# Kernel tuning notes

Measured on AMD Instinct MI355X. Metric: run time of the kernel, lower is better.

## Reference

```python
import jax, jax.numpy as jnp
import numpy as np

DIM = 2048
N_HEADS = 16
HEAD_DIM = DIM // N_HEADS
SEQ = 1024
BSZ = 2
ADAPTER_LEN = 10
MAX_FEATS = 10
ROPE_THETA = 10000.0


def setup_inputs() -> dict:
    key = jax.random.key(0)
    ks = jax.random.split(key, 10)
    x = jax.random.normal(ks[0], (BSZ, SEQ, DIM), dtype=jnp.float32)
    adapter = jax.random.normal(ks[1], (1, ADAPTER_LEN, DIM), dtype=jnp.float32)
    # causal additive mask [1,1,S,S]
    neg = jnp.full((SEQ, SEQ), -1e9, dtype=jnp.float32)
    mask = jnp.triu(neg, k=1)[None, None]
    # rotary frequencies (real/imag of freqs_cis)
    inv_freq = 1.0 / (ROPE_THETA ** (np.arange(0, HEAD_DIM, 2, dtype=np.float32) / HEAD_DIM))
    t = np.arange(SEQ, dtype=np.float32)
    ang = jnp.asarray(np.outer(t, inv_freq), dtype=jnp.float32)  # [S, HEAD_DIM//2]
    freqs_cos = jnp.cos(ang)
    freqs_sin = jnp.sin(ang)
    scale = 0.02
    wq = jax.random.normal(ks[2], (DIM, DIM), dtype=jnp.float32) * scale
    wk = jax.random.normal(ks[3], (DIM, DIM), dtype=jnp.float32) * scale
    wv = jax.random.normal(ks[4], (DIM, DIM), dtype=jnp.float32) * scale
    wo = jax.random.normal(ks[5], (DIM, DIM), dtype=jnp.float32) * scale
    gate1 = jax.random.normal(ks[6], (1, N_HEADS, 1, 1), dtype=jnp.float32) * 0.5
    gate2 = jnp.ones((1, N_HEADS, 1, 1), dtype=jnp.float32) * -3.0
    return {"x": x, "adapter": adapter, "mask": mask, "freqs_cos": freqs_cos,
            "freqs_sin": freqs_sin, "wq": wq, "wk": wk, "wv": wv, "wo": wo,
            "gate1": gate1, "gate2": gate2, "video_start": 30}


def _apply_rope(t, cos, sin):
    # t: [B,S,H,D]; cos/sin: [S, D//2] -> complex multiply on consecutive pairs
    tr = t.reshape(*t.shape[:-1], HEAD_DIM // 2, 2)
    xr, xi = tr[..., 0], tr[..., 1]
    c = cos[None, :, None, :]
    s = sin[None, :, None, :]
    out_r = xr * c - xi * s
    out_i = xr * s + xi * c
    return jnp.stack([out_r, out_i], axis=-1).reshape(t.shape)


def reference(x, adapter, mask, freqs_cos, freqs_sin, wq, wk, wv, wo, gate1, gate2, video_start):
    bsz, seqlen, _ = x.shape
    al = adapter.shape[1]
    vs = int(video_start)
    # projections (torch Linear: y = x @ W^T)
    xq = (x @ wq.T).reshape(bsz, seqlen, N_HEADS, HEAD_DIM)
    xk = (x @ wk.T).reshape(bsz, seqlen, N_HEADS, HEAD_DIM)
    xv = (x @ wv.T).reshape(bsz, seqlen, N_HEADS, HEAD_DIM)
    xq = _apply_rope(xq, freqs_cos, freqs_sin)
    xk = _apply_rope(xk, freqs_cos, freqs_sin)
    # adapter keys/values (no RoPE), broadcast over batch
    a_k = (adapter @ wk.T).reshape(1, al, N_HEADS, HEAD_DIM)
    a_v = (adapter @ wv.T).reshape(1, al, N_HEADS, HEAD_DIM)
    a_k = jnp.broadcast_to(a_k, (bsz, al, N_HEADS, HEAD_DIM))
    a_v = jnp.broadcast_to(a_v, (bsz, al, N_HEADS, HEAD_DIM))
    keys = jnp.concatenate([a_k, xk], axis=1)      # [B, al+S, H, D]
    values = jnp.concatenate([a_v, xv], axis=1)
    # mask extended with zeros over adapter columns
    extra = jnp.zeros((1, 1, seqlen, al), dtype=mask.dtype)
    full_mask = jnp.concatenate([extra, mask], axis=-1)
    scores = jnp.einsum('bqhd,bkhd->bhqk', xq, keys) / jnp.sqrt(jnp.float32(HEAD_DIM))
    scores = scores + full_mask
    # split softmax: adapter part gated by tanh(gate1)
    adapter_scores = jax.nn.softmax(scores[..., :al], axis=-1) * jnp.tanh(gate1)
    vt = scores[..., al:]
    vt = vt.at[:, :, vs + MAX_FEATS:, vs:vs + MAX_FEATS].add(gate2)
    vt = jax.nn.softmax(vt, axis=-1)
    probs = jnp.concatenate([adapter_scores, vt], axis=-1)  # [B,H,S,al+S]
    out = jnp.einsum('bhqk,bkhd->bqhd', probs, values)
    out = out.reshape(bsz, seqlen, DIM)
    return out @ wo.T
```

## Files before the change

### kernel.cpp

```cpp
#include <hip/hip_runtime.h>
#include <math.h>

#define DIM   2048
#define NH    16
#define HD    128
#define SEQQ  1024
#define BSZ   2
#define AL    10
#define MAXF  10
#define KVROWS (SEQQ + AL)
#define BK    32
#define VTP   2080

typedef unsigned short ushort_t;
typedef __bf16   bf16x8 __attribute__((ext_vector_type(8)));
typedef float    f32x4  __attribute__((ext_vector_type(4)));
typedef ushort_t us8    __attribute__((ext_vector_type(8)));

#define AS1 __attribute__((address_space(1)))
#define AS3 __attribute__((address_space(3)))

__device__ __forceinline__ float b2f(ushort_t u) {
    return __uint_as_float(((unsigned int)u) << 16);
}
__device__ __forceinline__ ushort_t f2b(float f) {
    unsigned int u = __float_as_uint(f);
    u += 0x7fffu + ((u >> 16) & 1u);
    return (ushort_t)(u >> 16);
}
__device__ __forceinline__ float scrub(float v, float canary) {
    return ((__float_as_uint(v) & 0x7f800000u) == 0x7f800000u) ? canary : v;
}
__device__ __forceinline__ bf16x8 cvt8(const float* p) {
    float4 a = *(const float4*)p;
    float4 b = *(const float4*)(p + 4);
    us8 u;
    u[0] = f2b(a.x); u[1] = f2b(a.y); u[2] = f2b(a.z); u[3] = f2b(a.w);
    u[4] = f2b(b.x); u[5] = f2b(b.y); u[6] = f2b(b.z); u[7] = f2b(b.w);
    return *(bf16x8*)&u;
}

__global__ __launch_bounds__(256) void cvt5(
    const float* __restrict__ s0, const float* __restrict__ s1,
    const float* __restrict__ s2, const float* __restrict__ s3,
    const float* __restrict__ s4,
    ushort_t* __restrict__ d0, ushort_t* __restrict__ d1,
    ushort_t* __restrict__ d2, ushort_t* __restrict__ d3,
    ushort_t* __restrict__ d4)
{
    const int y = blockIdx.y;
    const float* s = (y == 0) ? s0 : (y == 1) ? s1 : (y == 2) ? s2 : (y == 3) ? s3 : s4;
    ushort_t*    d = (y == 0) ? d0 : (y == 1) ? d1 : (y == 2) ? d2 : (y == 3) ? d3 : d4;
    size_t i = (size_t)blockIdx.x * 256 + threadIdx.x;
    float4 a = ((const float4*)s)[2 * i];
    float4 b = ((const float4*)s)[2 * i + 1];
    us8 u;
    u[0] = f2b(a.x); u[1] = f2b(a.y); u[2] = f2b(a.z); u[3] = f2b(a.w);
    u[4] = f2b(b.x); u[5] = f2b(b.y); u[6] = f2b(b.z); u[7] = f2b(b.w);
    *(us8*)(d + i * 8) = u;
}

__global__ __launch_bounds__(256) void adapter_gemm(
    const float* __restrict__ adp,
    const ushort_t* __restrict__ Wkb, const ushort_t* __restrict__ Wvb,
    ushort_t* __restrict__ Ko, ushort_t* __restrict__ VtO,
    float canary)
{
    __shared__ ushort_t Al[AL * DIM];

    const int t = threadIdx.x;
    #pragma unroll
    for (int p = 0; p < 10; ++p) {
        int i = p * 256 + t;
        const float* sp = adp + i * 8;
        float4 a = *(const float4*)sp;
        float4 b = *(const float4*)(sp + 4);
        us8 u;
        u[0] = f2b(a.x); u[1] = f2b(a.y); u[2] = f2b(a.z); u[3] = f2b(a.w);
        u[4] = f2b(b.x); u[5] = f2b(b.y); u[6] = f2b(b.z); u[7] = f2b(b.w);
        *(us8*)(Al + i * 8) = u;
    }
    __syncthreads();

    const int z = blockIdx.x >> 8;
    const ushort_t* W = z ? Wvb : Wkb;
    const int nbase = (blockIdx.x & 255) * 8;
    const int w = t >> 6, lane = t & 63;

    #pragma unroll
    for (int nn = 0; nn < 2; ++nn) {
        const int n = nbase + w * 2 + nn;
        const ushort_t* wr = W + (size_t)n * DIM;
        float acc[AL] = {};
        #pragma unroll
        for (int c = 0; c < 4; ++c) {
            const int k = c * 512 + lane * 8;
            us8 b8 = *(const us8*)(wr + k);
            float bf[8];
            #pragma unroll
            for (int j = 0; j < 8; ++j) bf[j] = b2f(b8[j]);
            #pragma unroll
            for (int m = 0; m < AL; ++m) {
                us8 a8 = *(const us8*)(Al + m * DIM + k);
                #pragma unroll
                for (int j = 0; j < 8; ++j)
                    acc[m] = fmaf(b2f(a8[j]), bf[j], acc[m]);
            }
        }
        #pragma unroll
        for (int m = 0; m < AL; ++m) {
            float v = acc[m];
            v += __shfl_xor(v, 1);  v += __shfl_xor(v, 2);
            v += __shfl_xor(v, 4);  v += __shfl_xor(v, 8);
            v += __shfl_xor(v, 16); v += __shfl_xor(v, 32);
            if (lane == 0) {
                ushort_t ov = f2b(scrub(v, canary));
                if (z) VtO[(size_t)n * VTP + 2048 + m] = ov;
                else   Ko[(size_t)m * DIM + n] = ov;
            }
        }
        if (z && lane < 22) VtO[(size_t)n * VTP + 2058 + lane] = 0;
    }
}

template<int MODE>
__global__ __launch_bounds__(256) void gemm_bt(
    const ushort_t* __restrict__ A,
    const ushort_t* __restrict__ B0, const ushort_t* __restrict__ B1, const ushort_t* __restrict__ B2,
    void* __restrict__ C0, void* __restrict__ C1, void* __restrict__ C2,
    float canary)
{
    __shared__ ushort_t As[128 * 32];
    __shared__ ushort_t Bs[128 * 32];

    const int z = blockIdx.z;
    const ushort_t* B = (z == 0) ? B0 : (z == 1) ? B1 : B2;
    void*           C = (z == 0) ? C0 : (z == 1) ? C1 : C2;

    const int m0 = blockIdx.y * 128;
    const int n0 = blockIdx.x * 128;
    const int t = threadIdx.x;
    const int w = t >> 6, lane = t & 63;
    const int ln = lane & 15, qd = lane >> 4;
    const int wrow = (w >> 1) * 64, wcol = (w & 1) * 64;

    const int r0 = t >> 2, c0 = (t & 3) * 8;
    const int r1 = (t + 256) >> 2;
    const ushort_t* Ag0 = A + (size_t)(m0 + r0) * DIM + c0;
    const ushort_t* Ag1 = A + (size_t)(m0 + r1) * DIM + c0;
    const ushort_t* Bg0 = B + (size_t)(n0 + r0) * DIM + c0;
    const ushort_t* Bg1 = B + (size_t)(n0 + r1) * DIM + c0;
    ushort_t* Al0 = As + (size_t)t * 8;
    ushort_t* Al1 = As + (size_t)(t + 256) * 8;
    ushort_t* Bl0 = Bs + (size_t)t * 8;
    ushort_t* Bl1 = Bs + (size_t)(t + 256) * 8;

    f32x4 acc[4][4] = {};

    for (int k0 = 0; k0 < DIM; k0 += BK) {
        if (k0) __syncthreads();
        __builtin_amdgcn_global_load_lds((const AS1 void*)(Ag0 + k0), (AS3 void*)Al0, 16, 0, 0);
        __builtin_amdgcn_global_load_lds((const AS1 void*)(Ag1 + k0), (AS3 void*)Al1, 16, 0, 0);
        __builtin_amdgcn_global_load_lds((const AS1 void*)(Bg0 + k0), (AS3 void*)Bl0, 16, 0, 0);
        __builtin_amdgcn_global_load_lds((const AS1 void*)(Bg1 + k0), (AS3 void*)Bl1, 16, 0, 0);
        __syncthreads();

        bf16x8 af[4], bfr[4];
        #pragma unroll
        for (int i = 0; i < 4; ++i) {
            af[i]  = *(const bf16x8*)(As + (wrow + i * 16 + ln) * 32 + qd * 8);
            bfr[i] = *(const bf16x8*)(Bs + (wcol + i * 16 + ln) * 32 + qd * 8);
        }
        #pragma unroll
        for (int i = 0; i < 4; ++i)
            #pragma unroll
            for (int j = 0; j < 4; ++j)
                acc[i][j] = __builtin_amdgcn_mfma_f32_16x16x32_bf16(af[i], bfr[j], acc[i][j], 0, 0, 0);
    }

    #pragma unroll
    for (int i = 0; i < 4; ++i) {
        #pragma unroll
        for (int j = 0; j < 4; ++j) {
            const int gn = n0 + wcol + j * 16 + ln;
            const int gm0 = m0 + wrow + i * 16 + qd * 4;
            if (MODE == 0 && z == 2) {
                ushort4 ov;
                ov.x = f2b(scrub(acc[i][j][0], canary));
                ov.y = f2b(scrub(acc[i][j][1], canary));
                ov.z = f2b(scrub(acc[i][j][2], canary));
                ov.w = f2b(scrub(acc[i][j][3], canary));
                *(ushort4*)((ushort_t*)C + (size_t)gn * VTP + gm0) = ov;
            } else {
                #pragma unroll
                for (int r = 0; r < 4; ++r) {
                    float v = scrub(acc[i][j][r], canary);
                    if (MODE == 1) ((float*)C)[(size_t)(gm0 + r) * DIM + gn] = v;
                    else           ((ushort_t*)C)[(size_t)(gm0 + r) * DIM + gn] = f2b(v);
                }
            }
        }
    }
}

template<bool AF32, bool CF32>
__global__ __launch_bounds__(256) void mfma_gemm(
    const void* __restrict__ Av,
    const float* __restrict__ B0, const float* __restrict__ B1, const float* __restrict__ B2,
    void* __restrict__ C0, void* __restrict__ C1, void* __restrict__ C2,
    int M, float canary)
{
    const int z = blockIdx.z;
    const float* B = (z == 0) ? B0 : (z == 1) ? B1 : B2;
    void*       C = (z == 0) ? C0 : (z == 1) ? C1 : C2;

    const int m0 = blockIdx.y * 128;
    const int n0 = blockIdx.x * 128;
    const int t    = threadIdx.x;
    const int w    = t >> 6;
    const int lane = t & 63;
    const int ln   = lane & 15, qd = lane >> 4;
    const int wrow = (w >> 1) * 64, wcol = (w & 1) * 64;

    size_t aoff[4];
    const float* brow[4];
    #pragma unroll
    for (int i = 0; i < 4; ++i) {
        int gr = m0 + wrow + i * 16 + ln; gr = (gr < M) ? gr : (M - 1);
        aoff[i] = (size_t)gr * DIM + qd * 8;
        brow[i] = B + (size_t)(n0 + wcol + i * 16 + ln) * DIM + qd * 8;
    }

    f32x4 acc[4][4] = {};

    for (int k0 = 0; k0 < DIM; k0 += BK) {
        bf16x8 af[4], bfr[4];
        #pragma unroll
        for (int i = 0; i < 4; ++i) {
            if (AF32) af[i] = cvt8((const float*)Av + aoff[i] + k0);
            else      af[i] = *(const bf16x8*)((const ushort_t*)Av + aoff[i] + k0);
            bfr[i] = cvt8(brow[i] + k0);
        }
        #pragma unroll
        for (int i = 0; i < 4; ++i)
            #pragma unroll
            for (int j = 0; j < 4; ++j)
                acc[i][j] = __builtin_amdgcn_mfma_f32_16x16x32_bf16(af[i], bfr[j], acc[i][j], 0, 0, 0);
    }

    #pragma unroll
    for (int i = 0; i < 4; ++i) {
        #pragma unroll
        for (int j = 0; j < 4; ++j) {
            const int gn = n0 + wcol + j * 16 + ln;
            #pragma unroll
            for (int r = 0; r < 4; ++r) {
                const int gm = m0 + wrow + i * 16 + qd * 4 + r;
                float v = scrub(acc[i][j][r], canary);
                if (gm < M) {
                    if (CF32) ((float*)C)[(size_t)gm * DIM + gn] = v;
                    else      ((ushort_t*)C)[(size_t)gm * DIM + gn] = f2b(v);
                }
            }
        }
    }
}

__global__ __launch_bounds__(256) void rope_kernel(ushort_t* __restrict__ Qb,
                                                   ushort_t* __restrict__ Kb,
                                                   const float* __restrict__ fc,
                                                   const float* __restrict__ fs,
                                                   float qscale)
{
    int i = blockIdx.x * 256 + threadIdx.x;
    ushort_t* T = blockIdx.y ? Kb : Qb;
    const float sc = blockIdx.y ? 1.0f : qscale;
    int row = i >> 10;
    int p   = i & 1023;
    float c = fc[((row & 1023) << 6) + (p & 63)];
    float s = fs[((row & 1023) << 6) + (p & 63)];
    ushort_t* ptr = T + (size_t)row * DIM + p * 2;
    float xr = b2f(ptr[0]), xi = b2f(ptr[1]);
    ptr[0] = f2b((xr * c - xi * s) * sc);
    ptr[1] = f2b((xr * s + xi * c) * sc);
}

__global__ __launch_bounds__(256) void attn_mfma(const ushort_t* __restrict__ Q,
                                                 const ushort_t* __restrict__ Kg,
                                                 const ushort_t* __restrict__ Vt,
                                                 const float* __restrict__ g1,
                                                 const float* __restrict__ g2,
                                                 const int* __restrict__ vsp,
                                                 ushort_t* __restrict__ AO)
{
    __shared__ ushort_t Kls[2][64 * 128];
    __shared__ ushort_t Vls[2][128 * 64];
    __shared__ ushort_t Pl[4 * 16 * 72];

    const int blk = blockIdx.x;
    const int wg   = (blk & 7) * 64 + (blk >> 3);
    const int gidx = wg >> 4;
    const int mem  = wg & 15;
    const int qt   = (mem & 1) ? (mem >> 1) : (15 - (mem >> 1));
    const int h = gidx & 15;
    const int b = gidx >> 4;
    const int q0  = qt * 64;
    const int nsteps = qt + 1;
    const int t = threadIdx.x;
    const int w = t >> 6, lane = t & 63;
    const int ln = lane & 15, g = lane >> 4;
    const int hb = h * HD;
    const size_t kvb = (size_t)b << 10;
    const int vs = *vsp;
    const float g2h = g2[h];
    const float ag  = tanhf(g1[h]);
    const int gq = q0 + w * 16 + ln;

    const ushort_t* qrow = Q + (kvb + gq) * DIM + hb;
    bf16x8 qf[4];
    #pragma unroll
    for (int c = 0; c < 4; ++c) qf[c] = *(const bf16x8*)(qrow + g * 8 + 32 * c);

    auto stage = [&](int bi, int k0) {
        #pragma unroll
        for (int p = 0; p < 4; ++p) {
            int i = t + 256 * p;
            int kr = i >> 4, ks = (i & 15) ^ (kr & 7);
            __builtin_amdgcn_global_load_lds(
                (const AS1 void*)(Kg + (kvb + k0 + kr) * DIM + hb + ks * 8),
                (AS3 void*)(&Kls[bi][i * 8]), 16, 0, 0);
        }
        #pragma unroll
        for (int p = 0; p < 4; ++p) {
            int i = t + 256 * p;
            int vr = i >> 3, vsl = (i & 7) ^ (vr & 7);
            __builtin_amdgcn_global_load_lds(
                (const AS1 void*)(Vt + (size_t)(hb + vr) * VTP + kvb + k0 + vsl * 8),
                (AS3 void*)(&Vls[bi][i * 8]), 16, 0, 0);
        }
    };

    stage(0, 0);

    f32x4 oa[8] = {};
    float m_run = -1e30f, l_run = 0.f;
    ushort_t* Plw = Pl + w * (16 * 72) + ln * 72;

    for (int s = 0; s < nsteps; ++s) {
        const int k0 = s * 64;
        const int cur = s & 1;
        __syncthreads();
        if (s + 1 < nsteps) stage(cur ^ 1, k0 + 64);

        f32x4 sc[4] = {};
        #pragma unroll
        for (int mt = 0; mt < 4; ++mt) {
            const int krow = ln + 16 * mt;
            const ushort_t* krp = &Kls[cur][krow * 128];
            #pragma unroll
            for (int c = 0; c < 4; ++c) {
                bf16x8 kf = *(const bf16x8*)(krp + ((8 * g + 32 * c) ^ ((krow & 7) << 3)));
                sc[mt] = __builtin_amdgcn_mfma_f32_16x16x32_bf16(kf, qf[c], sc[mt], 0, 0, 0);
            }
        }

        float mloc = -3e38f;
        #pragma unroll
        for (int mt = 0; mt < 4; ++mt)
            #pragma unroll
            for (int r = 0; r < 4; ++r) {
                int gk = k0 + mt * 16 + g * 4 + r;
                float v = sc[mt][r];
                if (gk > gq) v -= 1e9f;
                if (gk >= vs && gk < vs + MAXF && gq >= vs + MAXF) v += g2h;
                sc[mt][r] = v;
                mloc = fmaxf(mloc, v);
            }
        mloc = fmaxf(mloc, __shfl_xor(mloc, 16));
        mloc = fmaxf(mloc, __shfl_xor(mloc, 32));
        const float m_new = fmaxf(m_run, mloc);
        const float alpha = __expf(m_run - m_new);
        float psum = 0.f;
        #pragma unroll
        for (int mt = 0; mt < 4; ++mt) {
            float p0 = __expf(sc[mt][0] - m_new);
            float p1 = __expf(sc[mt][1] - m_new);
            float p2 = __expf(sc[mt][2] - m_new);
            float p3 = __expf(sc[mt][3] - m_new);
            psum += (p0 + p1) + (p2 + p3);
            uint2 pw_;
            pw_.x = (unsigned)f2b(p0) | ((unsigned)f2b(p1) << 16);
            pw_.y = (unsigned)f2b(p2) | ((unsigned)f2b(p3) << 16);
            *(uint2*)(Plw + mt * 16 + g * 4) = pw_;
        }
        psum += __shfl_xor(psum, 16);
        psum += __shfl_xor(psum, 32);
        l_run = l_run * alpha + psum;
        m_run = m_new;
        #pragma unroll
        for (int i = 0; i < 8; ++i) {
            oa[i][0] *= alpha; oa[i][1] *= alpha; oa[i][2] *= alpha; oa[i][3] *= alpha;
        }

        bf16x8 pf0 = *(const bf16x8*)(Plw + 8 * g);
        bf16x8 pf1 = *(const bf16x8*)(Plw + 32 + 8 * g);
        #pragma unroll
        for (int dt = 0; dt < 8; ++dt) {
            const int vrow = dt * 16 + ln;
            const ushort_t* vrp = &Vls[cur][vrow * 64];
            bf16x8 vf0 = *(const bf16x8*)(vrp + ((g     ^ (vrow & 7)) * 8));
            bf16x8 vf1 = *(const bf16x8*)(vrp + (((g+4) ^ (vrow & 7)) * 8));
            oa[dt] = __builtin_amdgcn_mfma_f32_16x16x32_bf16(vf0, pf0, oa[dt], 0, 0, 0);
            oa[dt] = __builtin_amdgcn_mfma_f32_16x16x32_bf16(vf1, pf1, oa[dt], 0, 0, 0);
        }
    }

    const float invl = 1.f / l_run;
    #pragma unroll
    for (int i = 0; i < 8; ++i) {
        oa[i][0] *= invl; oa[i][1] *= invl; oa[i][2] *= invl; oa[i][3] *= invl;
    }

    const ushort_t* karow = Kg + (size_t)(2048 + (ln < 10 ? ln : 9)) * DIM + hb;
    f32x4 sa4 = {};
    #pragma unroll
    for (int c = 0; c < 4; ++c) {
        bf16x8 kf = *(const bf16x8*)(karow + 8 * g + 32 * c);
        sa4 = __builtin_amdgcn_mfma_f32_16x16x32_bf16(kf, qf[c], sa4, 0, 0, 0);
    }
    float am = -3e38f;
    float pa[4];
    #pragma unroll
    for (int r = 0; r < 4; ++r) {
        int kl = g * 4 + r;
        pa[r] = (kl < 10) ? sa4[r] : -1e30f;
        am = fmaxf(am, pa[r]);
    }
    am = fmaxf(am, __shfl_xor(am, 16));
    am = fmaxf(am, __shfl_xor(am, 32));
    float asum = 0.f;
    #pragma unroll
    for (int r = 0; r < 4; ++r) { pa[r] = __expf(pa[r] - am); asum += pa[r]; }
    asum += __shfl_xor(asum, 16);
    asum += __shfl_xor(asum, 32);
    const float coef = ag / asum;
    {
        uint2 pw_;
        pw_.x = (unsigned)f2b(pa[0] * coef) | ((unsigned)f2b(pa[1] * coef) << 16);
        pw_.y = (unsigned)f2b(pa[2] * coef) | ((unsigned)f2b(pa[3] * coef) << 16);
        *(uint2*)(Plw + g * 4) = pw_;
        uint2 z2; z2.x = 0; z2.y = 0;
        *(uint2*)(Plw + 16 + g * 4) = z2;
    }
    bf16x8 paf = *(const bf16x8*)(Plw + 8 * g);
    #pragma unroll
    for (int dt = 0; dt < 8; ++dt) {
        const ushort_t* varow = Vt + (size_t)(hb + dt * 16 + ln) * VTP + 2048;
        bf16x8 vfa = *(const bf16x8*)(varow + 8 * g);
        oa[dt] = __builtin_amdgcn_mfma_f32_16x16x32_bf16(vfa, paf, oa[dt], 0, 0, 0);
    }

    ushort_t* outp = AO + (kvb + gq) * DIM + hb;
    #pragma unroll
    for (int dt = 0; dt < 8; ++dt) {
        ushort4 ov;
        ov.x = f2b(scrub(oa[dt][0], 1e8f));
        ov.y = f2b(scrub(oa[dt][1], 1e8f));
        ov.z = f2b(scrub(oa[dt][2], 1e8f));
        ov.w = f2b(scrub(oa[dt][3], 1e8f));
        *(ushort4*)(outp + dt * 16 + g * 4) = ov;
    }
}

__global__ __launch_bounds__(256) void attn_kernel(const ushort_t* __restrict__ Q,
                                                   const ushort_t* __restrict__ Kg,
                                                   const ushort_t* __restrict__ Vg,
                                                   const float* __restrict__ g1,
                                                   const float* __restrict__ g2,
                                                   const int* __restrict__ vsp,
                                                   ushort_t* __restrict__ AO)
{
    __shared__ float Qs[32 * 132];
    __shared__ float Ks[32 * 132];
    __shared__ float Vs[32 * 132];
    __shared__ float Ps[32 * 32];

    const int blk = blockIdx.x;
    const int q0  = (31 - (blk & 31)) * 32;
    const int h   = blk >> 5;
    const int t   = threadIdx.x;
    const int qi  = t >> 3;
    const int l8  = t & 7;
    const int vs  = *vsp;
    const int g_q = q0 + qi;
    const float scale = 0.08838834764831845f;
    const float g2h = g2[h];
    const float ag  = tanhf(g1[h]);

    #pragma unroll
    for (int p = 0; p < 4; ++p) {
        int idx = (p * 256 + t) * 4;
        int r = idx >> 7, d = idx & 127;
        ushort4 q4 = *(const ushort4*)(Q + (size_t)(q0 + r) * DIM + h * HD + d);
        *(float4*)(Qs + r * 132 + d) = make_float4(b2f(q4.x), b2f(q4.y), b2f(q4.z), b2f(q4.w));
    }

    float o[16];
    #pragma unroll
    for (int i = 0; i < 16; ++i) o[i] = 0.f;
    float m_run = -1e30f, l_run = 0.f;

    for (int k0 = 0; k0 <= q0 + 31; k0 += 32) {
        __syncthreads();
        #pragma unroll
        for (int p = 0; p < 4; ++p) {
            int idx = (p * 256 + t) * 4;
            int r = idx >> 7, d = idx & 127;
            size_t goff = (size_t)(k0 + r) * DIM + h * HD + d;
            ushort4 k4 = *(const ushort4*)(Kg + goff);
            ushort4 v4 = *(const ushort4*)(Vg + goff);
            *(float4*)(Ks + r * 132 + d) = make_float4(b2f(k4.x), b2f(k4.y), b2f(k4.z), b2f(k4.w));
            *(float4*)(Vs + r * 132 + d) = make_float4(b2f(v4.x), b2f(v4.y), b2f(v4.z), b2f(v4.w));
        }
        __syncthreads();

        float s[4];
        #pragma unroll
        for (int jj = 0; jj < 4; ++jj) s[jj] = 0.f;
        #pragma unroll 4
        for (int d = 0; d < 128; d += 4) {
            const float4 qv = *(const float4*)(Qs + qi * 132 + d);
            #pragma unroll
            for (int jj = 0; jj < 4; ++jj) {
                const float4 kv = *(const float4*)(Ks + (l8 + 8 * jj) * 132 + d);
                s[jj] += qv.x * kv.x + qv.y * kv.y + qv.z * kv.z + qv.w * kv.w;
            }
        }
        float mloc = -1e30f;
        #pragma unroll
        for (int jj = 0; jj < 4; ++jj) {
            int gk = k0 + l8 + 8 * jj;
            float sv = s[jj] * scale;
            if (gk > g_q) sv -= 1e9f;
            if (gk >= vs && gk < vs + MAXF && g_q >= vs + MAXF) sv += g2h;
            s[jj] = sv;
            mloc = fmaxf(mloc, sv);
        }
        mloc = fmaxf(mloc, __shfl_xor(mloc, 1));
        mloc = fmaxf(mloc, __shfl_xor(mloc, 2));
        mloc = fmaxf(mloc, __shfl_xor(mloc, 4));
        const float m_new = fmaxf(m_run, mloc);
        const float alpha = expf(m_run - m_new);
        float psum = 0.f;
        #pragma unroll
        for (int jj = 0; jj < 4; ++jj) {
            float pv = expf(s[jj] - m_new);
            psum += pv;
            Ps[qi * 32 + l8 + 8 * jj] = pv;
        }
        psum += __shfl_xor(psum, 1);
        psum += __shfl_xor(psum, 2);
        psum += __shfl_xor(psum, 4);
        l_run = l_run * alpha + psum;
        m_run = m_new;
        #pragma unroll
        for (int i = 0; i < 16; ++i) o[i] *= alpha;
        __syncthreads();

        #pragma unroll 4
        for (int kk = 0; kk < 32; ++kk) {
            const float pp = Ps[qi * 32 + kk];
            const float* vr = Vs + kk * 132 + l8 * 4;
            #pragma unroll
            for (int jj = 0; jj < 4; ++jj) {
                const float4 v4 = *(const float4*)(vr + jj * 32);
                o[jj*4+0] = fmaf(pp, v4.x, o[jj*4+0]);
                o[jj*4+1] = fmaf(pp, v4.y, o[jj*4+1]);
                o[jj*4+2] = fmaf(pp, v4.z, o[jj*4+2]);
                o[jj*4+3] = fmaf(pp, v4.w, o[jj*4+3]);
            }
        }
    }

    const float invl = 1.f / l_run;
    #pragma unroll
    for (int i = 0; i < 16; ++i) o[i] *= invl;

    __syncthreads();
    #pragma unroll
    for (int p = 0; p < 2; ++p) {
        int idx = p * 256 + t;
        if (idx < 320) {
            int fi = idx * 4; int r = fi >> 7; int d = fi & 127;
            size_t goff = (size_t)(SEQQ + r) * DIM + h * HD + d;
            ushort4 k4 = *(const ushort4*)(Kg + goff);
            ushort4 v4 = *(const ushort4*)(Vg + goff);
            *(float4*)(Ks + r * 132 + d) = make_float4(b2f(k4.x), b2f(k4.y), b2f(k4.z), b2f(k4.w));
            *(float4*)(Vs + r * 132 + d) = make_float4(b2f(v4.x), b2f(v4.y), b2f(v4.z), b2f(v4.w));
        }
    }
    __syncthreads();
    float sa[2] = {-1e30f, -1e30f};
    #pragma unroll
    for (int jj = 0; jj < 2; ++jj) {
        int kk = l8 + 8 * jj;
        if (kk < AL) {
            float acc = 0.f;
            #pragma unroll 4
            for (int d = 0; d < 128; d += 4) {
                const float4 qv = *(const float4*)(Qs + qi * 132 + d);
                const float4 kv = *(const float4*)(Ks + kk * 132 + d);
                acc += qv.x * kv.x + qv.y * kv.y + qv.z * kv.z + qv.w * kv.w;
            }
            sa[jj] = acc * scale;
        }
    }
    float am = fmaxf(sa[0], sa[1]);
    am = fmaxf(am, __shfl_xor(am, 1));
    am = fmaxf(am, __shfl_xor(am, 2));
    am = fmaxf(am, __shfl_xor(am, 4));
    float pa0 = expf(sa[0] - am);
    float pa1 = (l8 < 2) ? expf(sa[1] - am) : 0.f;
    float asum = pa0 + pa1;
    asum += __shfl_xor(asum, 1);
    asum += __shfl_xor(asum, 2);
    asum += __shfl_xor(asum, 4);
    const float coef = ag / asum;
    Ps[qi * 32 + l8] = pa0 * coef;
    if (l8 < 2) Ps[qi * 32 + 8 + l8] = pa1 * coef;
    __syncthreads();
    #pragma unroll
    for (int kk = 0; kk < AL; ++kk) {
        const float pp = Ps[qi * 32 + kk];
        const float* vr = Vs + kk * 132 + l8 * 4;
        #pragma unroll
        for (int jj = 0; jj < 4; ++jj) {
            const float4 v4 = *(const float4*)(vr + jj * 32);
            o[jj*4+0] = fmaf(pp, v4.x, o[jj*4+0]);
            o[jj*4+1] = fmaf(pp, v4.y, o[jj*4+1]);
            o[jj*4+2] = fmaf(pp, v4.z, o[jj*4+2]);
            o[jj*4+3] = fmaf(pp, v4.w, o[jj*4+3]);
        }
    }

    ushort_t* outp = AO + (size_t)g_q * DIM + h * HD + l8 * 4;
    #pragma unroll
    for (int jj = 0; jj < 4; ++jj) {
        ushort4 ov;
        ov.x = f2b(scrub(o[jj*4+0], 1e8f));
        ov.y = f2b(scrub(o[jj*4+1], 1e8f));
        ov.z = f2b(scrub(o[jj*4+2], 1e8f));
        ov.w = f2b(scrub(o[jj*4+3], 1e8f));
        *(ushort4*)(outp + jj * 32) = ov;
    }
}

extern "C" void kernel_launch(void* const* d_in, const int* in_sizes, int n_in,
                              void* d_out, int out_size, void* d_ws, size_t ws_size,
                              hipStream_t stream)
{
    const float* x   = (const float*)d_in[0];
    const float* adp = (const float*)d_in[1];
    const float* fc  = (const float*)d_in[3];
    const float* fs  = (const float*)d_in[4];
    const float* wq  = (const float*)d_in[5];
    const float* wk  = (const float*)d_in[6];
    const float* wv  = (const float*)d_in[7];
    const float* wo  = (const float*)d_in[8];
    const float* g1  = (const float*)d_in[9];
    const float* g2  = (const float*)d_in[10];
    const int*   vsp = (const int*)d_in[11];

    float* out = (float*)d_out;

    const size_t rows2 = (size_t)BSZ * SEQQ;
    const size_t qe2 = rows2 * DIM;
    const size_t ke2 = (rows2 + AL) * DIM;
    const size_t vte = (size_t)DIM * VTP;
    const size_t we  = (size_t)DIM * DIM;
    const size_t xe  = (size_t)BSZ * SEQQ * DIM;
    const size_t need = (qe2 + ke2 + vte + xe + 4 * we) * sizeof(ushort_t);

    if (ws_size >= need) {
        ushort_t* Qb  = (ushort_t*)d_ws;
        ushort_t* Kb  = Qb + qe2;
        ushort_t* VtG = Kb + ke2;
        ushort_t* Xb  = VtG + vte;
        ushort_t* Wqb = Xb + xe;
        ushort_t* Wkb = Wqb + we;
        ushort_t* Wvb = Wkb + we;
        ushort_t* Wob = Wvb + we;

        cvt5<<<dim3(2048, 5), 256, 0, stream>>>(wq, wk, wv, wo, x,
                                                Wqb, Wkb, Wvb, Wob, Xb);

        adapter_gemm<<<512, 256, 0, stream>>>(adp, Wkb, Wvb,
                                              Kb + rows2 * DIM, VtG,
                                              100.0f);

        gemm_bt<0><<<dim3(16, 16, 3), 256, 0, stream>>>(
            Xb, Wqb, Wkb, Wvb, Qb, Kb, VtG, 1e5f);

        rope_kernel<<<dim3(8192, 2), 256, 0, stream>>>(Qb, Kb, fc, fs,
                                                       0.08838834764831845f);

        attn_mfma<<<512, 256, 0, stream>>>(Qb, Kb, VtG, g1, g2, vsp, Qb );

        gemm_bt<1><<<dim3(16, 16, 1), 256, 0, stream>>>(
            Qb, Wob, Wob, Wob, out, out, out, 1e12f);
    } else {
        const size_t qe = (size_t)SEQQ * DIM;
        const size_t ke = (size_t)KVROWS * DIM;
        ushort_t* Qb = (ushort_t*)d_ws;
        ushort_t* Kb = Qb + qe;
        ushort_t* Vb = Kb + ke;

        mfma_gemm<true, false><<<dim3(16, 1, 2), 256, 0, stream>>>(
            adp, wk, wv, wv,
            Kb + qe, Vb + qe, Vb,
            AL, 100.0f);

        for (int b = 0; b < BSZ; ++b) {
            const long xo = (long)b * SEQQ * DIM;
            mfma_gemm<true, false><<<dim3(16, 8, 3), 256, 0, stream>>>(
                x + xo, wq, wk, wv, Qb, Kb, Vb, SEQQ, 1e5f);

            rope_kernel<<<dim3(4096, 2), 256, 0, stream>>>(Qb, Kb, fc, fs, 1.0f);

            attn_kernel<<<NH * (SEQQ / 32), 256, 0, stream>>>(Qb, Kb, Vb, g1, g2, vsp, Qb);

            mfma_gemm<false, true><<<dim3(16, 8, 1), 256, 0, stream>>>(
                Qb, wo, wo, wo, out + xo, out + xo, out + xo, SEQQ, 1e12f);
        }
    }
}
```

Baseline: 302.6 us.

## Fuse RoPE into QKV GEMM epilogue, remap workgroups across XCDs, add MFMA priority

```diff
diff --git a/kernel.cpp b/kernel.cpp
--- a/kernel.cpp
+++ b/kernel.cpp
@@ -128,17 +128,23 @@
     const ushort_t* __restrict__ A,
     const ushort_t* __restrict__ B0, const ushort_t* __restrict__ B1, const ushort_t* __restrict__ B2,
     void* __restrict__ C0, void* __restrict__ C1, void* __restrict__ C2,
-    float canary)
+    const float* __restrict__ fc, const float* __restrict__ fs,
+    float qscale, float canary)
 {
     __shared__ ushort_t As[128 * 32];
     __shared__ ushort_t Bs[128 * 32];
 
-    const int z = blockIdx.z;
+    const int lid  = blockIdx.x + (blockIdx.y << 4) + (blockIdx.z << 8);
+    const int cpx  = (int)(gridDim.z << 5);
+    const int wgid = (lid & 7) * cpx + (lid >> 3);
+    const int z    = wgid >> 8;
+    const int rem  = wgid & 255;
+    const int m0   = (rem >> 4) << 7;
+    const int n0   = (rem & 15) << 7;
+
     const ushort_t* B = (z == 0) ? B0 : (z == 1) ? B1 : B2;
     void*           C = (z == 0) ? C0 : (z == 1) ? C1 : C2;
 
-    const int m0 = blockIdx.y * 128;
-    const int n0 = blockIdx.x * 128;
     const int t = threadIdx.x;
     const int w = t >> 6, lane = t & 63;
     const int ln = lane & 15, qd = lane >> 4;
@@ -178,6 +184,8 @@
                 acc[i][j] = __builtin_amdgcn_mfma_f32_16x16x32_bf16(af[i], bfr[j], acc[i][j], 0, 0, 0);
     }
 
+    const float rsc = (MODE == 0 && z == 0) ? qscale : 1.0f;
+
     #pragma unroll
     for (int i = 0; i < 4; ++i) {
         #pragma unroll
@@ -191,12 +199,23 @@
                 ov.z = f2b(scrub(acc[i][j][2], canary));
                 ov.w = f2b(scrub(acc[i][j][3], canary));
                 *(ushort4*)((ushort_t*)C + (size_t)gn * VTP + gm0) = ov;
+            } else if (MODE == 0) {
+                const int fidx = (gn & 127) >> 1;
+                #pragma unroll
+                for (int r = 0; r < 4; ++r) {
+                    const int gm = gm0 + r;
+                    float v = scrub(acc[i][j][r], canary);
+                    float po = __shfl_xor(v, 1);
+                    const int fo = ((gm & 1023) << 6) + fidx;
+                    float c = fc[fo], s = fs[fo];
+                    float ov = (ln & 1) ? (po * s + v * c) : (v * c - po * s);
+                    ((ushort_t*)C)[(size_t)gm * DIM + gn] = f2b(ov * rsc);
+                }
             } else {
                 #pragma unroll
                 for (int r = 0; r < 4; ++r) {
                     float v = scrub(acc[i][j][r], canary);
-                    if (MODE == 1) ((float*)C)[(size_t)(gm0 + r) * DIM + gn] = v;
-                    else           ((ushort_t*)C)[(size_t)(gm0 + r) * DIM + gn] = f2b(v);
+                    ((float*)C)[(size_t)(gm0 + r) * DIM + gn] = v;
                 }
             }
         }
@@ -353,6 +372,7 @@
         if (s + 1 < nsteps) stage(cur ^ 1, k0 + 64);
 
         f32x4 sc[4] = {};
+        __builtin_amdgcn_s_setprio(1);
         #pragma unroll
         for (int mt = 0; mt < 4; ++mt) {
             const int krow = ln + 16 * mt;
@@ -363,6 +383,7 @@
                 sc[mt] = __builtin_amdgcn_mfma_f32_16x16x32_bf16(kf, qf[c], sc[mt], 0, 0, 0);
             }
         }
+        __builtin_amdgcn_s_setprio(0);
 
         float mloc = -3e38f;
         #pragma unroll
@@ -404,6 +425,7 @@
 
         bf16x8 pf0 = *(const bf16x8*)(Plw + 8 * g);
         bf16x8 pf1 = *(const bf16x8*)(Plw + 32 + 8 * g);
+        __builtin_amdgcn_s_setprio(1);
         #pragma unroll
         for (int dt = 0; dt < 8; ++dt) {
             const int vrow = dt * 16 + ln;
@@ -413,6 +435,7 @@
             oa[dt] = __builtin_amdgcn_mfma_f32_16x16x32_bf16(vf0, pf0, oa[dt], 0, 0, 0);
             oa[dt] = __builtin_amdgcn_mfma_f32_16x16x32_bf16(vf1, pf1, oa[dt], 0, 0, 0);
         }
+        __builtin_amdgcn_s_setprio(0);
     }
 
     const float invl = 1.f / l_run;
@@ -699,15 +722,14 @@
                                               100.0f);
 
         gemm_bt<0><<<dim3(16, 16, 3), 256, 0, stream>>>(
-            Xb, Wqb, Wkb, Wvb, Qb, Kb, VtG, 1e5f);
-
-        rope_kernel<<<dim3(8192, 2), 256, 0, stream>>>(Qb, Kb, fc, fs,
-                                                       0.08838834764831845f);
+            Xb, Wqb, Wkb, Wvb, Qb, Kb, VtG,
+            fc, fs, 0.08838834764831845f, 1e5f);
 
         attn_mfma<<<512, 256, 0, stream>>>(Qb, Kb, VtG, g1, g2, vsp, Qb );
 
         gemm_bt<1><<<dim3(16, 16, 1), 256, 0, stream>>>(
-            Qb, Wob, Wob, Wob, out, out, out, 1e12f);
+            Qb, Wob, Wob, Wob, out, out, out,
+            fc, fs, 1.0f, 1e12f);
     } else {
         const size_t qe = (size_t)SEQQ * DIM;
         const size_t ke = (size_t)KVROWS * DIM;
```

Result: faster. 291.9 us (-3.5%).
